# Kernel tuning notes

Measured on AMD Instinct MI355X. Metric: run time of the kernel, lower is better.

The kernel has to match this reference:

```python
import jax, jax.numpy as jnp
import numpy as np

DIM = 512
NUM_HEADS = 8
HEAD_DIM = DIM // NUM_HEADS
SCALE = HEAD_DIM ** -0.5
B, T = 8, 1024


def setup_inputs() -> dict:
    key = jax.random.key(0)
    ks = jax.random.split(key, 6)
    x = jax.random.normal(ks[0], (B, T, DIM), dtype=jnp.float32)
    attn_mask = jax.random.randint(ks[1], (B, T, T), 0, 2) == 1  # bool [B,T,T]
    s = 1.0 / np.sqrt(DIM)
    qkv_w = jax.random.uniform(ks[2], (3 * DIM, DIM), jnp.float32, -s, s)
    qkv_b = jax.random.uniform(ks[3], (3 * DIM,), jnp.float32, -s, s)
    proj_w = jax.random.uniform(ks[4], (DIM, DIM), jnp.float32, -s, s)
    proj_b = jax.random.uniform(ks[5], (DIM,), jnp.float32, -s, s)
    return {"x": x, "attn_mask": attn_mask, "qkv_w": qkv_w, "qkv_b": qkv_b,
            "proj_w": proj_w, "proj_b": proj_b}


def reference(x, attn_mask, qkv_w, qkv_b, proj_w, proj_b):
    b, t, c = x.shape
    # QKV projection (torch Linear: x @ W.T + b), split into q,k,v heads
    qkv = x @ qkv_w.T + qkv_b                      # [b,t,3*c]
    qkv = qkv.reshape(b, t, 3, NUM_HEADS, HEAD_DIM)
    qkv = jnp.transpose(qkv, (2, 0, 3, 1, 4))      # [3,b,h,t,d]
    q, k, v = qkv[0], qkv[1], qkv[2]
    scores = jnp.einsum('bhqd,bhkd->bhqk', q, k) * SCALE  # [b,h,t,t]
    min_val = jnp.finfo(scores.dtype).min
    scores = jnp.where(attn_mask[:, None, :, :], min_val, scores)
    attn = jax.nn.softmax(scores, axis=-1)
    out = jnp.einsum('bhqk,bhkd->bhqd', attn, v)   # [b,h,t,d]
    out = jnp.transpose(out, (0, 2, 1, 3)).reshape(b, t, c)
    return out @ proj_w.T + proj_b
```

## Files before the change

kernel.cpp:

```cpp
#include <hip/hip_runtime.h>
#include <math.h>

#define DIM   512
#define NH    8
#define HD    64
#define BATCH 8
#define SEQ   1024
#define SCALE 0.125f
#define MINV  (-3.402823466e38f)

typedef unsigned short u16;
typedef unsigned int   u32;
typedef unsigned long long u64;
typedef __bf16 bf16x8 __attribute__((ext_vector_type(8)));
typedef float  f32x4  __attribute__((ext_vector_type(4)));

__device__ inline u16 f2bf(float f) {
  u32 u = __builtin_bit_cast(u32, f);
  return (u16)((u + 0x7fffu + ((u >> 16) & 1u)) >> 16);
}
__device__ inline float bf2f(u16 h) {
  return __builtin_bit_cast(float, (u32)h << 16);
}

__device__ inline void a16(const u16* g, u16* l) {
  __builtin_amdgcn_global_load_lds(
      (const __attribute__((address_space(1))) u32*)g,
      (__attribute__((address_space(3))) u32*)l, 16, 0, 0);
}


__global__ __launch_bounds__(256) void pack_mask(const int* __restrict__ mask,
                                                 u64* __restrict__ bits) {
  const size_t gid = (size_t)blockIdx.x * 256 + threadIdx.x;
  const int lane = threadIdx.x & 63;
  const size_t word = gid >> 6;
  const int v = mask[word * 64 + lane];
  const u64 b = __ballot(v != 0);
  if (lane == 0) bits[word] = b;
}

__global__ __launch_bounds__(256) void decompose(const float* __restrict__ src,
                                                 u16* __restrict__ hi,
                                                 u16* __restrict__ lo) {
  const int rg = blockIdx.x;
  const int t = threadIdx.x;
  const float* s = src + (size_t)rg * 16 * DIM;
  u16* ph = hi + (size_t)rg * 8192;
  u16* pl = lo + (size_t)rg * 8192;
  #pragma unroll
  for (int c = 0; c < 4; ++c) {
    const int cid = c * 256 + t;
    const int row = cid & 15, kc = cid >> 4;
    float f[8];
    *(float4*)&f[0] = *(const float4*)&s[row * DIM + kc * 8];
    *(float4*)&f[4] = *(const float4*)&s[row * DIM + kc * 8 + 4];
    u16 hv[8], lv[8];
    #pragma unroll
    for (int j = 0; j < 8; ++j) {
      hv[j] = f2bf(f[j]);
      lv[j] = f2bf(f[j] - bf2f(hv[j]));
    }
    *(uint4*)&ph[(size_t)cid * 8] = *(const uint4*)hv;
    *(uint4*)&pl[(size_t)cid * 8] = *(const uint4*)lv;
  }
}

template <bool QKV>
__global__ __launch_bounds__(256) void mfma_gemm(
    const u16* __restrict__ Agh, const u16* __restrict__ Agl,
    const u16* __restrict__ Bgh, const u16* __restrict__ Bgl,
    const float* __restrict__ bias, void* __restrict__ out0,
    u16* __restrict__ kb, u16* __restrict__ vb) {
  __shared__ u16 sAh[4096];
  __shared__ u16 sAl[4096];
  __shared__ u16 sBh[4096];
  __shared__ u16 sBl[4096];

  const int tid = threadIdx.x;
  const int lane = tid & 63;
  const int wv = tid >> 6;
  const int lk = lane & 15, lq = lane >> 4;
  const int n0 = blockIdx.x * 128, m0 = blockIdx.y * 128;
  const int wm = (wv & 1) * 4;
  const int wn = (wv >> 1) * 4;

  const u16* gAh = Agh + (size_t)(m0 >> 4) * 8192 + lane * 8;
  const u16* gAl = Agl + (size_t)(m0 >> 4) * 8192 + lane * 8;
  const u16* gBh = Bgh + (size_t)(n0 >> 4) * 8192 + lane * 8;
  const u16* gBl = Bgl + (size_t)(n0 >> 4) * 8192 + lane * 8;

  f32x4 acc[4][4];
  #pragma unroll
  for (int i = 0; i < 4; ++i)
    #pragma unroll
    for (int j = 0; j < 4; ++j) acc[i][j] = (f32x4){0.f, 0.f, 0.f, 0.f};

  #pragma unroll 1
  for (int ki = 0; ki < 16; ++ki) {
    __syncthreads();
    #pragma unroll
    for (int it = 0; it < 2; ++it) {
      const int t = it * 4 + wv;
      const size_t go = (size_t)t * 8192 + ki * 512;
      const int lo_ = t * 512 + lane * 8;
      a16(gAh + go, &sAh[lo_]);
      a16(gAl + go, &sAl[lo_]);
      a16(gBh + go, &sBh[lo_]);
      a16(gBl + go, &sBl[lo_]);
    }
    __syncthreads();

    bf16x8 ah[4], al[4], bh[4], bl[4];
    #pragma unroll
    for (int i = 0; i < 4; ++i) {
      ah[i] = *(const bf16x8*)&sAh[(wm + i) * 512 + lane * 8];
      al[i] = *(const bf16x8*)&sAl[(wm + i) * 512 + lane * 8];
      bh[i] = *(const bf16x8*)&sBh[(wn + i) * 512 + lane * 8];
      bl[i] = *(const bf16x8*)&sBl[(wn + i) * 512 + lane * 8];
    }
    #pragma unroll
    for (int i = 0; i < 4; ++i)
      #pragma unroll
      for (int j = 0; j < 4; ++j) {
        acc[i][j] = __builtin_amdgcn_mfma_f32_16x16x32_bf16(ah[i], bh[j], acc[i][j], 0, 0, 0);
        acc[i][j] = __builtin_amdgcn_mfma_f32_16x16x32_bf16(ah[i], bl[j], acc[i][j], 0, 0, 0);
        acc[i][j] = __builtin_amdgcn_mfma_f32_16x16x32_bf16(al[i], bh[j], acc[i][j], 0, 0, 0);
      }
  }

  #pragma unroll
  for (int j = 0; j < 4; ++j) {
    const int n = n0 + (wn + j) * 16 + lk;
    const float bv = bias[n];
    #pragma unroll
    for (int i = 0; i < 4; ++i) {
      #pragma unroll
      for (int r = 0; r < 4; ++r) {
        const int m = m0 + (wm + i) * 16 + lq * 4 + r;
        const float v = acc[i][j][r] + bv;
        if (QKV) {
          const int which = n >> 9, h = (n >> 6) & 7, d = n & 63;
          u16* dst = (which == 0) ? (u16*)out0 : (which == 1) ? kb : vb;
          const int b = m >> 10, tok = m & 1023;
          dst[(((size_t)((b << 3) + h) << 10 | tok) << 6) + d] = f2bf(v);
        } else {
          ((float*)out0)[(size_t)m * DIM + n] = v;
        }
      }
    }
  }
}

__global__ __launch_bounds__(256, 4) void attn_mfma(
    const u16* __restrict__ qg, const u16* __restrict__ kg,
    const u16* __restrict__ vg, const u64* __restrict__ bits,
    u16* __restrict__ ohi, u16* __restrict__ olo) {
  __shared__ u16 Qs[64 * 72];
  __shared__ u16 Ks[64 * 72];
  __shared__ u16 VT[64 * 72];
  __shared__ u16 Ps[64 * 72];
  __shared__ u64 msk[64];

  const int tid  = threadIdx.x;
  const int lane = tid & 63;
  const int wv   = tid >> 6;
  const int lk   = lane & 15;
  const int lq   = lane >> 4;
  const int q0   = blockIdx.x * 64;
  const int bh   = blockIdx.y;
  const int bb   = bh >> 3;

  #pragma unroll
  for (int it = 0; it < 2; ++it) {
    const int idx = it * 256 + tid;
    const int t = idx >> 3, d0 = (idx & 7) * 8;
    *(uint4*)&Qs[t * 72 + d0] =
        *(const uint4*)&qg[((size_t)(bh << 10 | (q0 + t)) << 6) + d0];
  }
  __syncthreads();

  const bf16x8 aq0 = *(const bf16x8*)&Qs[(size_t)(wv * 16 + lk) * 72 + lq * 8];
  const bf16x8 aq1 = *(const bf16x8*)&Qs[(size_t)(wv * 16 + lk) * 72 + 32 + lq * 8];

  f32x4 o_[4];
  float m_i[4], l_i[4];
  #pragma unroll
  for (int r = 0; r < 4; ++r) { m_i[r] = MINV; l_i[r] = 0.f; }
  #pragma unroll
  for (int t = 0; t < 4; ++t) o_[t] = (f32x4){0.f, 0.f, 0.f, 0.f};

  #pragma unroll 1
  for (int kt = 0; kt < SEQ / 64; ++kt) {
    __syncthreads();

    #pragma unroll
    for (int it = 0; it < 2; ++it) {
      const int idx = it * 256 + tid;
      const int t = idx >> 3, d0 = (idx & 7) * 8;
      *(uint4*)&Ks[t * 72 + d0] =
          *(const uint4*)&kg[((size_t)(bh << 10 | (kt * 64 + t)) << 6) + d0];
    }
    {
      const int kp = tid & 31, d0 = (tid >> 5) * 8;
      const int k = 2 * kp;
      const u16* s0 = &vg[((size_t)(bh << 10 | (kt * 64 + k)) << 6) + d0];
      u16 a[8], b[8];
      *(uint4*)a = *(const uint4*)s0;
      *(uint4*)b = *(const uint4*)(s0 + 64);
      #pragma unroll
      for (int j = 0; j < 8; ++j)
        *(u32*)&VT[(size_t)(d0 + j) * 72 + k] = (u32)a[j] | ((u32)b[j] << 16);
    }
    if (tid < 64)
      msk[tid] = bits[((size_t)(bb << 10 | (q0 + tid)) << 4) + kt];
    __syncthreads();

    f32x4 s[4];
    const f32x4 zero = (f32x4){0.f, 0.f, 0.f, 0.f};
    #pragma unroll
    for (int t = 0; t < 4; ++t) {
      const bf16x8 bk0 = *(const bf16x8*)&Ks[(size_t)(t * 16 + lk) * 72 + lq * 8];
      const bf16x8 bk1 = *(const bf16x8*)&Ks[(size_t)(t * 16 + lk) * 72 + 32 + lq * 8];
      f32x4 acc = __builtin_amdgcn_mfma_f32_16x16x32_bf16(aq0, bk0, zero, 0, 0, 0);
      s[t] = __builtin_amdgcn_mfma_f32_16x16x32_bf16(aq1, bk1, acc, 0, 0, 0);
    }

    #pragma unroll
    for (int r = 0; r < 4; ++r) {
      const int qrow = wv * 16 + lq * 4 + r;
      const u64 wd = msk[qrow];
      float sv[4];
      #pragma unroll
      for (int t = 0; t < 4; ++t)
        sv[t] = ((wd >> (t * 16 + lk)) & 1ull) ? MINV : s[t][r] * SCALE;
      float tm = fmaxf(fmaxf(sv[0], sv[1]), fmaxf(sv[2], sv[3]));
      #pragma unroll
      for (int o = 8; o; o >>= 1) tm = fmaxf(tm, __shfl_xor(tm, o));
      const float mn = fmaxf(m_i[r], tm);
      const float alpha = __expf(m_i[r] - mn);
      float rs = 0.f;
      #pragma unroll
      for (int t = 0; t < 4; ++t) {
        const float pv = __expf(sv[t] - mn);
        rs += pv;
        Ps[(size_t)qrow * 72 + t * 16 + lk] = f2bf(pv);
      }
      #pragma unroll
      for (int o = 8; o; o >>= 1) rs += __shfl_xor(rs, o);
      l_i[r] = l_i[r] * alpha + rs;
      m_i[r] = mn;
      #pragma unroll
      for (int t = 0; t < 4; ++t) o_[t][r] *= alpha;
    }

    const bf16x8 pa0 = *(const bf16x8*)&Ps[(size_t)(wv * 16 + lk) * 72 + lq * 8];
    const bf16x8 pa1 = *(const bf16x8*)&Ps[(size_t)(wv * 16 + lk) * 72 + 32 + lq * 8];
    #pragma unroll
    for (int t = 0; t < 4; ++t) {
      const bf16x8 vb0 = *(const bf16x8*)&VT[(size_t)(t * 16 + lk) * 72 + lq * 8];
      const bf16x8 vb1 = *(const bf16x8*)&VT[(size_t)(t * 16 + lk) * 72 + 32 + lq * 8];
      o_[t] = __builtin_amdgcn_mfma_f32_16x16x32_bf16(pa0, vb0, o_[t], 0, 0, 0);
      o_[t] = __builtin_amdgcn_mfma_f32_16x16x32_bf16(pa1, vb1, o_[t], 0, 0, 0);
    }
  }

  const int b = bh >> 3, h = bh & 7;
  #pragma unroll
  for (int r = 0; r < 4; ++r) {
    const float inv = 1.0f / l_i[r];
    const int tok = q0 + wv * 16 + lq * 4 + r;
    const int m = (b << 10) | tok;
    const size_t rgo = (size_t)(m >> 4) * 8192 + (size_t)(m & 15) * 8;
    #pragma unroll
    for (int t = 0; t < 4; ++t) {
      const int d = t * 16 + lk;
      const int k = (h << 6) | d;
      const float v = o_[t][r] * inv;
      const u16 hv = f2bf(v);
      const size_t off = rgo + (size_t)(k >> 3) * 128 + (k & 7);
      ohi[off] = hv;
      olo[off] = f2bf(v - bf2f(hv));
    }
  }
}

extern "C" void kernel_launch(void* const* d_in, const int* in_sizes, int n_in,
                              void* d_out, int out_size, void* d_ws,
                              size_t ws_size, hipStream_t stream) {
  const float* x      = (const float*)d_in[0];
  const int*   mask   = (const int*)d_in[1];
  const float* qkv_w  = (const float*)d_in[2];
  const float* qkv_b  = (const float*)d_in[3];
  const float* proj_w = (const float*)d_in[4];
  const float* proj_b = (const float*)d_in[5];
  float* out = (float*)d_out;

  const size_t SZ = (size_t)BATCH * NH * SEQ * HD;
  u64* bits = (u64*)d_ws;
  u16* qb  = (u16*)(bits + 131072);
  u16* kb  = qb + SZ;
  u16* vb  = kb + SZ;
  u16* xhi = vb + SZ;
  u16* xlo = xhi + SZ;
  u16* ohi = xlo + SZ;
  u16* olo = ohi + SZ;
  u16* wqh = olo + SZ;
  u16* wql = wqh + 1536 * 512;
  u16* wph = wql + 1536 * 512;
  u16* wpl = wph + 512 * 512;

  pack_mask<<<(BATCH * SEQ * SEQ) / 256, 256, 0, stream>>>(mask, bits);
  decompose<<<8192 / 16, 256, 0, stream>>>(x, xhi, xlo);
  decompose<<<1536 / 16, 256, 0, stream>>>(qkv_w, wqh, wql);
  decompose<<<512 / 16, 256, 0, stream>>>(proj_w, wph, wpl);

  mfma_gemm<true><<<dim3(12, 64), 256, 0, stream>>>(
      xhi, xlo, wqh, wql, qkv_b, qb, kb, vb);
  attn_mfma<<<dim3(SEQ / 64, BATCH * NH), 256, 0, stream>>>(
      qb, kb, vb, bits, ohi, olo);
  mfma_gemm<false><<<dim3(4, 64), 256, 0, stream>>>(
      ohi, olo, wph, wpl, proj_b, out, nullptr, nullptr);
}
```

Measured before the change: 244.0 us.

## Drop online max in attention, prescale Q, transpose V and mask, skip LDS staging

Q is pre-scaled by SCALE·log2(e) in the QKV GEMM epilogue, V is written transposed, and the mask bits are stored key-tile-major. Together these let the attention kernel load K, V and mask straight from global memory into registers, with no shared-memory staging and no block barriers. Softmax now uses exp2 without a running max, which removes the max reductions, the rescaling of the accumulator and the shuffles per tile, and the row sum is reduced only once at the end. The risk is that skipping max subtraction can overflow for large scores, and a fully masked row now gives 0/0 instead of the reference's uniform weights.

```diff
diff --git a/kernel.cpp b/kernel.cpp
--- a/kernel.cpp
+++ b/kernel.cpp
@@ -6,8 +6,7 @@
 #define HD    64
 #define BATCH 8
 #define SEQ   1024
-#define SCALE 0.125f
-#define MINV  (-3.402823466e38f)
+#define QSCALE 0.18033688011112042f
 
 typedef unsigned short u16;
 typedef unsigned int   u32;
@@ -22,6 +21,9 @@
 __device__ inline float bf2f(u16 h) {
   return __builtin_bit_cast(float, (u32)h << 16);
 }
+__device__ inline u32 pk2(float a, float b) {
+  return (u32)f2bf(a) | ((u32)f2bf(b) << 16);
+}
 
 __device__ inline void a16(const u16* g, u16* l) {
   __builtin_amdgcn_global_load_lds(
@@ -34,10 +36,13 @@
                                                  u64* __restrict__ bits) {
   const size_t gid = (size_t)blockIdx.x * 256 + threadIdx.x;
   const int lane = threadIdx.x & 63;
-  const size_t word = gid >> 6;
-  const int v = mask[word * 64 + lane];
+  const size_t w = gid >> 6;
+  const int v = mask[w * 64 + lane];
   const u64 b = __ballot(v != 0);
-  if (lane == 0) bits[word] = b;
+  if (lane == 0) {
+    const int bb = (int)(w >> 14), q = (int)((w >> 4) & 1023), kt = (int)(w & 15);
+    bits[(((size_t)(bb << 4 | kt)) << 10) | q] = b;
+  }
 }
 
 __global__ __launch_bounds__(256) void decompose(const float* __restrict__ src,
@@ -71,7 +76,7 @@
     const u16* __restrict__ Agh, const u16* __restrict__ Agl,
     const u16* __restrict__ Bgh, const u16* __restrict__ Bgl,
     const float* __restrict__ bias, void* __restrict__ out0,
-    u16* __restrict__ kb, u16* __restrict__ vb) {
+    u16* __restrict__ kb, u16* __restrict__ vtb) {
   __shared__ u16 sAh[4096];
   __shared__ u16 sAl[4096];
   __shared__ u16 sBh[4096];
@@ -132,145 +137,121 @@
   #pragma unroll
   for (int j = 0; j < 4; ++j) {
     const int n = n0 + (wn + j) * 16 + lk;
-    const float bv = bias[n];
+    const float bv_ = bias[n];
     #pragma unroll
     for (int i = 0; i < 4; ++i) {
+      const int mb = m0 + (wm + i) * 16 + lq * 4;
+      if (QKV) {
+        const int which = n >> 9, h = (n >> 6) & 7, d = n & 63;
+        const int b = mb >> 10, tok0 = mb & 1023;
+        if (which == 2) {
+          ushort4 o;
+          o.x = f2bf(acc[i][j][0] + bv_);
+          o.y = f2bf(acc[i][j][1] + bv_);
+          o.z = f2bf(acc[i][j][2] + bv_);
+          o.w = f2bf(acc[i][j][3] + bv_);
+          *(ushort4*)&vtb[(((size_t)((b << 3) + h) << 6 | d) << 10) + tok0] = o;
+        } else {
+          u16* dst = which ? kb : (u16*)out0;
+          const float sc = which ? 1.0f : QSCALE;
+          #pragma unroll
+          for (int r = 0; r < 4; ++r)
+            dst[(((size_t)((b << 3) + h) << 10 | (tok0 + r)) << 6) + d] =
+                f2bf((acc[i][j][r] + bv_) * sc);
+        }
+      } else {
+        #pragma unroll
+        for (int r = 0; r < 4; ++r)
+          ((float*)out0)[(size_t)(mb + r) * DIM + n] = acc[i][j][r] + bv_;
+      }
+    }
+  }
+}
+
+__global__ __launch_bounds__(256) void attn_mfma(
+    const u16* __restrict__ qg, const u16* __restrict__ kg,
+    const u16* __restrict__ vtg, const u64* __restrict__ bitsT,
+    u16* __restrict__ ohi, u16* __restrict__ olo) {
+  __shared__ u16 Ps[64 * 72];
+
+  const int tid = threadIdx.x;
+  const int lane = tid & 63;
+  const int wv = tid >> 6;
+  const int lk = lane & 15, lq = lane >> 4;
+  const int q0 = blockIdx.x * 64;
+  const int bh = blockIdx.y;
+  const int bb = bh >> 3;
+  const int q = q0 + wv * 16 + lk;
+
+  const u16* qrow = qg + ((size_t)(bh << 10 | q) << 6);
+  const bf16x8 bq0 = *(const bf16x8*)(qrow + lq * 8);
+  const bf16x8 bq1 = *(const bf16x8*)(qrow + 32 + lq * 8);
+
+  const u16* kbase = kg + ((size_t)bh << 16) + ((size_t)lk << 6) + lq * 8;
+  const u16* vbase = vtg + ((size_t)bh << 16) + ((size_t)lk << 10) + lq * 8;
+  const u64* bitp = bitsT + ((size_t)bb << 14) + q;
+  u16* pw = &Ps[(wv * 16 + lk) * 72];
+
+  f32x4 o_[4];
+  float l = 0.f;
+  #pragma unroll
+  for (int t = 0; t < 4; ++t) o_[t] = (f32x4){0.f, 0.f, 0.f, 0.f};
+
+  #pragma unroll 1
+  for (int kt = 0; kt < 16; ++kt) {
+    bf16x8 ak[4][2], bv[4][2];
+    #pragma unroll
+    for (int t = 0; t < 4; ++t) {
+      const u16* kp = kbase + (size_t)((kt * 64 + t * 16) << 6);
+      ak[t][0] = *(const bf16x8*)kp;
+      ak[t][1] = *(const bf16x8*)(kp + 32);
+      const u16* vp = vbase + ((size_t)(t * 16) << 10) + kt * 64;
+      bv[t][0] = *(const bf16x8*)vp;
+      bv[t][1] = *(const bf16x8*)(vp + 32);
+    }
+    const u64 wd = bitp[kt << 10];
+    const u32 w0 = (u32)wd, w1 = (u32)(wd >> 32);
+
+    f32x4 st[4];
+    const f32x4 z4 = (f32x4){0.f, 0.f, 0.f, 0.f};
+    #pragma unroll
+    for (int t = 0; t < 4; ++t) {
+      f32x4 a = __builtin_amdgcn_mfma_f32_16x16x32_bf16(ak[t][0], bq0, z4, 0, 0, 0);
+      st[t] = __builtin_amdgcn_mfma_f32_16x16x32_bf16(ak[t][1], bq1, a, 0, 0, 0);
+    }
+
+    #pragma unroll
+    for (int t = 0; t < 4; ++t) {
+      const u32 w = (t < 2) ? w0 : w1;
+      const int base = (t & 1) * 16 + lq * 4;
+      float p[4];
       #pragma unroll
       for (int r = 0; r < 4; ++r) {
-        const int m = m0 + (wm + i) * 16 + lq * 4 + r;
-        const float v = acc[i][j][r] + bv;
-        if (QKV) {
-          const int which = n >> 9, h = (n >> 6) & 7, d = n & 63;
-          u16* dst = (which == 0) ? (u16*)out0 : (which == 1) ? kb : vb;
-          const int b = m >> 10, tok = m & 1023;
-          dst[(((size_t)((b << 3) + h) << 10 | tok) << 6) + d] = f2bf(v);
-        } else {
-          ((float*)out0)[(size_t)m * DIM + n] = v;
-        }
+        const float sv = ((w >> (base + r)) & 1u) ? -INFINITY : st[t][r];
+        p[r] = __builtin_amdgcn_exp2f(sv);
+        l += p[r];
       }
-    }
-  }
-}
-
-__global__ __launch_bounds__(256, 4) void attn_mfma(
-    const u16* __restrict__ qg, const u16* __restrict__ kg,
-    const u16* __restrict__ vg, const u64* __restrict__ bits,
-    u16* __restrict__ ohi, u16* __restrict__ olo) {
-  __shared__ u16 Qs[64 * 72];
-  __shared__ u16 Ks[64 * 72];
-  __shared__ u16 VT[64 * 72];
-  __shared__ u16 Ps[64 * 72];
-  __shared__ u64 msk[64];
-
-  const int tid  = threadIdx.x;
-  const int lane = tid & 63;
-  const int wv   = tid >> 6;
-  const int lk   = lane & 15;
-  const int lq   = lane >> 4;
-  const int q0   = blockIdx.x * 64;
-  const int bh   = blockIdx.y;
-  const int bb   = bh >> 3;
-
-  #pragma unroll
-  for (int it = 0; it < 2; ++it) {
-    const int idx = it * 256 + tid;
-    const int t = idx >> 3, d0 = (idx & 7) * 8;
-    *(uint4*)&Qs[t * 72 + d0] =
-        *(const uint4*)&qg[((size_t)(bh << 10 | (q0 + t)) << 6) + d0];
-  }
-  __syncthreads();
-
-  const bf16x8 aq0 = *(const bf16x8*)&Qs[(size_t)(wv * 16 + lk) * 72 + lq * 8];
-  const bf16x8 aq1 = *(const bf16x8*)&Qs[(size_t)(wv * 16 + lk) * 72 + 32 + lq * 8];
-
-  f32x4 o_[4];
-  float m_i[4], l_i[4];
-  #pragma unroll
-  for (int r = 0; r < 4; ++r) { m_i[r] = MINV; l_i[r] = 0.f; }
-  #pragma unroll
-  for (int t = 0; t < 4; ++t) o_[t] = (f32x4){0.f, 0.f, 0.f, 0.f};
-
-  #pragma unroll 1
-  for (int kt = 0; kt < SEQ / 64; ++kt) {
-    __syncthreads();
-
-    #pragma unroll
-    for (int it = 0; it < 2; ++it) {
-      const int idx = it * 256 + tid;
-      const int t = idx >> 3, d0 = (idx & 7) * 8;
-      *(uint4*)&Ks[t * 72 + d0] =
-          *(const uint4*)&kg[((size_t)(bh << 10 | (kt * 64 + t)) << 6) + d0];
-    }
-    {
-      const int kp = tid & 31, d0 = (tid >> 5) * 8;
-      const int k = 2 * kp;
-      const u16* s0 = &vg[((size_t)(bh << 10 | (kt * 64 + k)) << 6) + d0];
-      u16 a[8], b[8];
-      *(uint4*)a = *(const uint4*)s0;
-      *(uint4*)b = *(const uint4*)(s0 + 64);
-      #pragma unroll
-      for (int j = 0; j < 8; ++j)
-        *(u32*)&VT[(size_t)(d0 + j) * 72 + k] = (u32)a[j] | ((u32)b[j] << 16);
-    }
-    if (tid < 64)
-      msk[tid] = bits[((size_t)(bb << 10 | (q0 + tid)) << 4) + kt];
-    __syncthreads();
-
-    f32x4 s[4];
-    const f32x4 zero = (f32x4){0.f, 0.f, 0.f, 0.f};
-    #pragma unroll
-    for (int t = 0; t < 4; ++t) {
-      const bf16x8 bk0 = *(const bf16x8*)&Ks[(size_t)(t * 16 + lk) * 72 + lq * 8];
-      const bf16x8 bk1 = *(const bf16x8*)&Ks[(size_t)(t * 16 + lk) * 72 + 32 + lq * 8];
-      f32x4 acc = __builtin_amdgcn_mfma_f32_16x16x32_bf16(aq0, bk0, zero, 0, 0, 0);
-      s[t] = __builtin_amdgcn_mfma_f32_16x16x32_bf16(aq1, bk1, acc, 0, 0, 0);
-    }
-
-    #pragma unroll
-    for (int r = 0; r < 4; ++r) {
-      const int qrow = wv * 16 + lq * 4 + r;
-      const u64 wd = msk[qrow];
-      float sv[4];
-      #pragma unroll
-      for (int t = 0; t < 4; ++t)
-        sv[t] = ((wd >> (t * 16 + lk)) & 1ull) ? MINV : s[t][r] * SCALE;
-      float tm = fmaxf(fmaxf(sv[0], sv[1]), fmaxf(sv[2], sv[3]));
-      #pragma unroll
-      for (int o = 8; o; o >>= 1) tm = fmaxf(tm, __shfl_xor(tm, o));
-      const float mn = fmaxf(m_i[r], tm);
-      const float alpha = __expf(m_i[r] - mn);
-      float rs = 0.f;
-      #pragma unroll
-      for (int t = 0; t < 4; ++t) {
-        const float pv = __expf(sv[t] - mn);
-        rs += pv;
-        Ps[(size_t)qrow * 72 + t * 16 + lk] = f2bf(pv);
-      }
-      #pragma unroll
-      for (int o = 8; o; o >>= 1) rs += __shfl_xor(rs, o);
-      l_i[r] = l_i[r] * alpha + rs;
-      m_i[r] = mn;
-      #pragma unroll
-      for (int t = 0; t < 4; ++t) o_[t][r] *= alpha;
-    }
-
-    const bf16x8 pa0 = *(const bf16x8*)&Ps[(size_t)(wv * 16 + lk) * 72 + lq * 8];
-    const bf16x8 pa1 = *(const bf16x8*)&Ps[(size_t)(wv * 16 + lk) * 72 + 32 + lq * 8];
-    #pragma unroll
-    for (int t = 0; t < 4; ++t) {
-      const bf16x8 vb0 = *(const bf16x8*)&VT[(size_t)(t * 16 + lk) * 72 + lq * 8];
-      const bf16x8 vb1 = *(const bf16x8*)&VT[(size_t)(t * 16 + lk) * 72 + 32 + lq * 8];
-      o_[t] = __builtin_amdgcn_mfma_f32_16x16x32_bf16(pa0, vb0, o_[t], 0, 0, 0);
-      o_[t] = __builtin_amdgcn_mfma_f32_16x16x32_bf16(pa1, vb1, o_[t], 0, 0, 0);
-    }
-  }
-
-  const int b = bh >> 3, h = bh & 7;
+      *(uint2*)(pw + t * 16 + lq * 4) = uint2{pk2(p[0], p[1]), pk2(p[2], p[3])};
+    }
+
+    const bf16x8 pa0 = *(const bf16x8*)(pw + lq * 8);
+    const bf16x8 pa1 = *(const bf16x8*)(pw + 32 + lq * 8);
+    #pragma unroll
+    for (int t = 0; t < 4; ++t) {
+      o_[t] = __builtin_amdgcn_mfma_f32_16x16x32_bf16(pa0, bv[t][0], o_[t], 0, 0, 0);
+      o_[t] = __builtin_amdgcn_mfma_f32_16x16x32_bf16(pa1, bv[t][1], o_[t], 0, 0, 0);
+    }
+  }
+
+  l += __shfl_xor(l, 16);
+  l += __shfl_xor(l, 32);
+
+  const int h = bh & 7;
   #pragma unroll
   for (int r = 0; r < 4; ++r) {
-    const float inv = 1.0f / l_i[r];
+    const float inv = 1.0f / __shfl(l, lq * 4 + r);
     const int tok = q0 + wv * 16 + lq * 4 + r;
-    const int m = (b << 10) | tok;
+    const int m = (bb << 10) | tok;
     const size_t rgo = (size_t)(m >> 4) * 8192 + (size_t)(m & 15) * 8;
     #pragma unroll
     for (int t = 0; t < 4; ++t) {
@@ -300,8 +281,8 @@
   u64* bits = (u64*)d_ws;
   u16* qb  = (u16*)(bits + 131072);
   u16* kb  = qb + SZ;
-  u16* vb  = kb + SZ;
-  u16* xhi = vb + SZ;
+  u16* vtb = kb + SZ;
+  u16* xhi = vtb + SZ;
   u16* xlo = xhi + SZ;
   u16* ohi = xlo + SZ;
   u16* olo = ohi + SZ;
@@ -316,9 +297,9 @@
   decompose<<<512 / 16, 256, 0, stream>>>(proj_w, wph, wpl);
 
   mfma_gemm<true><<<dim3(12, 64), 256, 0, stream>>>(
-      xhi, xlo, wqh, wql, qkv_b, qb, kb, vb);
+      xhi, xlo, wqh, wql, qkv_b, qb, kb, vtb);
   attn_mfma<<<dim3(SEQ / 64, BATCH * NH), 256, 0, stream>>>(
-      qb, kb, vb, bits, ohi, olo);
+      qb, kb, vtb, bits, ohi, olo);
   mfma_gemm<false><<<dim3(4, 64), 256, 0, stream>>>(
       ohi, olo, wph, wpl, proj_b, out, nullptr, nullptr);
 }
```

Result: slower. 301.5 us (+23.5%).
